# Optimization experiments

Measured on AMD Instinct MI355X. Metric: run time of the kernel, lower is better.

The kernel has to match this reference:

```python
import jax, jax.numpy as jnp
import numpy as np

N, D, C = 8192, 512, 1000


def setup_inputs() -> dict:
    key = jax.random.key(0)
    k1, k2, k3 = jax.random.split(key, 3)
    features = jax.random.normal(k1, (N, D), dtype=jnp.float32)
    centers = jax.random.normal(k2, (C, D), dtype=jnp.float32)
    labels = jax.random.randint(k3, (N,), 0, C, dtype=jnp.int64)
    return {"features": features, "centers": centers, "labels": labels}


def _l2_normalize(x, axis=1, eps=1e-12):
    # matches torch F.normalize(p=2): x / max(||x||, eps)
    norm = jnp.sqrt(jnp.sum(x * x, axis=axis, keepdims=True))
    return x / jnp.maximum(norm, eps)


def reference(features, centers, labels):
    f = _l2_normalize(features, axis=1)          # [N, D]
    c = _l2_normalize(centers, axis=1)           # [C, D]
    centers_batch = c[labels]                    # [N, D]
    pos_distances = 1.0 - jnp.sum(f * centers_batch, axis=1)      # [N]
    neg_distances = 1.0 - jnp.matmul(f, f.T)                       # [N, N]
    losses = pos_distances[:, None] - neg_distances                # [N, N]
    diff_class = labels[:, None] != labels[None, :]                # [N, N]
    valid = diff_class & (losses > 0.0)                            # [N, N]
    losses = jnp.where(valid, losses, 0.0)
    num_valid_pairs = jnp.sum(valid, axis=1)                       # [N]
    num_valid_pairs = jnp.where(num_valid_pairs > 0, num_valid_pairs, 1)
    sample_losses = jnp.sum(losses, axis=1) / num_valid_pairs.astype(losses.dtype)
    num_valid_samples = jnp.sum(sample_losses > 0.0)
    loss = jnp.sum(sample_losses)
    loss = jnp.where(num_valid_samples > 0,
                     loss / num_valid_samples.astype(loss.dtype), loss)
    return loss
```

## Files before the change

### kernel.cpp

```cpp
#include <hip/hip_runtime.h>
#include <hip/hip_bf16.h>
#include <hip/hip_fp8.h>
#include <stdint.h>
#include <math.h>

#define N_ROWS 8192
#define DIM    512
#define BM     128
#define BK     64
#define NB     (N_ROWS / BM)
#define NTRI   (NB * (NB + 1) / 2)
#define NKT    (DIM / BK)

typedef float f32x4 __attribute__((ext_vector_type(4)));
typedef long  lng2  __attribute__((ext_vector_type(2)));


__global__ __launch_bounds__(256) void k_prep(const float* __restrict__ feats,
                                              const float* __restrict__ centers,
                                              const int* __restrict__ labels,
                                              unsigned char* __restrict__ f_q,
                                              float* __restrict__ posdot,
                                              float* __restrict__ Ssum,
                                              int* __restrict__ Kcnt) {
    const int row = blockIdx.x;
    const int t = threadIdx.x;
    const float* src = feats + (size_t)row * DIM;
    float v0 = src[t], v1 = src[t + 256];
    float ss = v0 * v0 + v1 * v1;
#pragma unroll
    for (int m = 1; m < 64; m <<= 1) ss += __shfl_xor(ss, m, 64);
    __shared__ float red[12];
    const int lane = t & 63, wid = t >> 6;
    if (lane == 0) red[wid] = ss;
    __syncthreads();
    const float tot = red[0] + red[1] + red[2] + red[3];
    const float scale = 1.0f / fmaxf(sqrtf(tot), 1e-12f);
    const float n0 = v0 * scale, n1 = v1 * scale;
    {
        __hip_fp8_e4m3 q0(n0), q1(n1);
#pragma unroll
        for (int j = 0; j < 2; ++j) {
            const int k  = t + j * 256;
            const int kt = k >> 6, k6 = k & 63;
            const int h  = (k6 >> 5) & 1;
            const int u  = (k6 >> 3) & 3;
            const int pos = kt * 64 + u * 16 + h * 8 + (k6 & 7);
            const unsigned char qb = (j == 0) ? *reinterpret_cast<const unsigned char*>(&q0)
                                              : *reinterpret_cast<const unsigned char*>(&q1);
            f_q[(size_t)row * DIM + pos] = qb;
        }
    }

    const int lab = labels[row];
    const float* c = centers + (size_t)lab * DIM;
    const float c0 = c[t], c1 = c[t + 256];
    float cc = c0 * c0 + c1 * c1;
    float d  = n0 * c0 + n1 * c1;
#pragma unroll
    for (int m = 1; m < 64; m <<= 1) {
        cc += __shfl_xor(cc, m, 64);
        d  += __shfl_xor(d, m, 64);
    }
    if (lane == 0) { red[4 + wid] = cc; red[8 + wid] = d; }
    __syncthreads();
    if (t == 0) {
        const float ctot = red[4] + red[5] + red[6] + red[7];
        const float dtot = red[8] + red[9] + red[10] + red[11];
        posdot[row] = dtot / fmaxf(sqrtf(ctot), 1e-12f);
        Ssum[row] = 0.0f;
        Kcnt[row] = 0;
    }
}

__global__ __launch_bounds__(256) void k_pair(const unsigned char* __restrict__ f_q,
                                              const int* __restrict__ labels,
                                              const float* __restrict__ pd,
                                              float* __restrict__ Ssum,
                                              int* __restrict__ Kcnt) {
    __shared__ __align__(16) unsigned char sA[2][BM * BK];
    __shared__ __align__(16) unsigned char sB[2][BM * BK];
    __shared__ int   s_lr[BM];
    __shared__ int   s_lc[BM];
    __shared__ float s_pd[BM];
    __shared__ float s_pc[BM];

    const int tid  = threadIdx.x;
    const int lane = tid & 63;
    const int wid  = tid >> 6;
    const int wr   = wid >> 1, wc = wid & 1;

    const int t = blockIdx.x;
    int bi = (int)floor((2.0 * NB + 1.0 - sqrt((2.0 * NB + 1.0) * (2.0 * NB + 1.0) - 8.0 * (double)t)) * 0.5);
    while (bi * NB - bi * (bi - 1) / 2 > t) --bi;
    while ((bi + 1) * NB - (bi + 1) * bi / 2 <= t) ++bi;
    const int bj = bi + (t - (bi * NB - bi * (bi - 1) / 2));
    const int rowBase = bi * BM;
    const int colBase = bj * BM;
    const bool offdiag = (bi != bj);

    if (tid < BM) {
        s_lr[tid] = labels[rowBase + tid];
        s_pd[tid] = pd[rowBase + tid];
    } else {
        s_lc[tid - BM] = labels[colBase + tid - BM];
        s_pc[tid - BM] = pd[colBase + tid - BM];
    }

    f32x4 acc[4][4] = {};

    const int srow = lane >> 2;
    const int slu  = (lane & 3) ^ ((lane >> 3) & 3);

#define STAGE(KT, P)                                                                       \
    do {                                                                                   \
        const int k0_ = (KT) * BK;                                                         \
        _Pragma("unroll")                                                                  \
        for (int i_ = 0; i_ < 2; ++i_) {                                                   \
            const int ch_ = wid * 2 + i_;                                                  \
            const int r_  = ch_ * 16 + srow;                                               \
            const unsigned char* gA_ = f_q + ((size_t)(rowBase + r_) * DIM + k0_ + slu * 16); \
            const unsigned char* gB_ = f_q + ((size_t)(colBase + r_) * DIM + k0_ + slu * 16); \
            __builtin_amdgcn_global_load_lds(                                              \
                (const __attribute__((address_space(1))) void*)gA_,                        \
                (__attribute__((address_space(3))) void*)(&sA[P][ch_ * 1024]), 16, 0, 0);  \
            __builtin_amdgcn_global_load_lds(                                              \
                (const __attribute__((address_space(1))) void*)gB_,                        \
                (__attribute__((address_space(3))) void*)(&sB[P][ch_ * 1024]), 16, 0, 0);  \
        }                                                                                  \
    } while (0)

    const int pu = (lane >> 4) ^ ((lane >> 1) & 3);

#define COMPUTE(P)                                                                         \
    do {                                                                                   \
        lng2 aF[4], bF[4];                                                                 \
        _Pragma("unroll")                                                                  \
        for (int m = 0; m < 4; ++m) {                                                      \
            const int r = wr * 64 + m * 16 + (lane & 15);                                  \
            aF[m] = *(const lng2*)(&sA[P][r * 64 + pu * 16]);                              \
        }                                                                                  \
        _Pragma("unroll")                                                                  \
        for (int n = 0; n < 4; ++n) {                                                      \
            const int r = wc * 64 + n * 16 + (lane & 15);                                  \
            bF[n] = *(const lng2*)(&sB[P][r * 64 + pu * 16]);                              \
        }                                                                                  \
        _Pragma("unroll")                                                                  \
        for (int m = 0; m < 4; ++m)                                                        \
            _Pragma("unroll")                                                              \
            for (int n = 0; n < 4; ++n) {                                                  \
                acc[m][n] = __builtin_amdgcn_mfma_f32_16x16x32_fp8_fp8(aF[m].x, bF[n].x, acc[m][n], 0, 0, 0); \
                acc[m][n] = __builtin_amdgcn_mfma_f32_16x16x32_fp8_fp8(aF[m].y, bF[n].y, acc[m][n], 0, 0, 0); \
            }                                                                              \
    } while (0)

    STAGE(0, 0);
    __syncthreads();

    for (int kt = 0; kt < NKT - 1; ++kt) {
        const int cur = kt & 1;
        STAGE(kt + 1, cur ^ 1);
        COMPUTE(cur);
        __syncthreads();
    }
    COMPUTE((NKT - 1) & 1);

#undef STAGE
#undef COMPUTE

    float colS[4] = {0.f, 0.f, 0.f, 0.f};
    int   colK[4] = {0, 0, 0, 0};
    int   lcv[4]; float pcv[4];
#pragma unroll
    for (int n = 0; n < 4; ++n) {
        const int jl = wc * 64 + n * 16 + (lane & 15);
        lcv[n] = s_lc[jl];
        pcv[n] = s_pc[jl];
    }

#pragma unroll
    for (int m = 0; m < 4; ++m) {
        float rowS[4] = {0.f, 0.f, 0.f, 0.f};
        int   rowK[4] = {0, 0, 0, 0};
        const int rbase = wr * 64 + m * 16 + ((lane >> 4) << 2);
        int myLr[4]; float myPd[4];
#pragma unroll
        for (int g = 0; g < 4; ++g) { myLr[g] = s_lr[rbase + g]; myPd[g] = s_pd[rbase + g]; }
#pragma unroll
        for (int n = 0; n < 4; ++n) {
#pragma unroll
            for (int g = 0; g < 4; ++g) {
                const float s = acc[m][n][g];
                const bool diff = (myLr[g] != lcv[n]);
                if (diff && s > myPd[g]) { rowS[g] += (s - myPd[g]); rowK[g] += 1; }
                if (offdiag && diff && s > pcv[n]) { colS[n] += (s - pcv[n]); colK[n] += 1; }
            }
        }
#pragma unroll
        for (int g = 0; g < 4; ++g) {
#pragma unroll
            for (int d = 1; d < 16; d <<= 1) {
                rowS[g] += __shfl_xor(rowS[g], d, 64);
                rowK[g] += __shfl_xor(rowK[g], d, 64);
            }
        }
        if ((lane & 15) == 0) {
#pragma unroll
            for (int g = 0; g < 4; ++g) {
                const int r = rowBase + rbase + g;
                atomicAdd(&Ssum[r], rowS[g]);
                atomicAdd(&Kcnt[r], rowK[g]);
            }
        }
    }

    if (offdiag) {
#pragma unroll
        for (int n = 0; n < 4; ++n) {
#pragma unroll
            for (int d = 16; d < 64; d <<= 1) {
                colS[n] += __shfl_xor(colS[n], d, 64);
                colK[n] += __shfl_xor(colK[n], d, 64);
            }
        }
        if (lane < 16) {
#pragma unroll
            for (int n = 0; n < 4; ++n) {
                const int c = colBase + wc * 64 + n * 16 + lane;
                atomicAdd(&Ssum[c], colS[n]);
                atomicAdd(&Kcnt[c], colK[n]);
            }
        }
    }
}

__global__ __launch_bounds__(1024) void k_final(const float* __restrict__ Ssum,
                                                const int* __restrict__ Kcnt,
                                                float* __restrict__ out) {
    const int t = threadIdx.x;
    double sum = 0.0; int cnt = 0;
    for (int i = t; i < N_ROWS; i += 1024) {
        const int k = Kcnt[i];
        if (k > 0) { sum += (double)Ssum[i] / (double)k; cnt += 1; }
    }
#pragma unroll
    for (int d = 1; d < 64; d <<= 1) {
        sum += __shfl_xor(sum, d, 64);
        cnt += __shfl_xor(cnt, d, 64);
    }
    __shared__ double s_sum[16];
    __shared__ int    s_cnt[16];
    const int lane = t & 63, wid = t >> 6;
    if (lane == 0) { s_sum[wid] = sum; s_cnt[wid] = cnt; }
    __syncthreads();
    if (t == 0) {
        double ts = 0.0; int tc = 0;
#pragma unroll
        for (int w = 0; w < 16; ++w) { ts += s_sum[w]; tc += s_cnt[w]; }
        out[0] = (float)(tc > 0 ? ts / (double)tc : ts);
    }
}

extern "C" void kernel_launch(void* const* d_in, const int* in_sizes, int n_in,
                              void* d_out, int out_size, void* d_ws, size_t ws_size,
                              hipStream_t stream) {
    const float* features = (const float*)d_in[0];
    const float* centers  = (const float*)d_in[1];
    const int*   labels   = (const int*)d_in[2];
    float* out = (float*)d_out;

    char* ws = (char*)d_ws;
    unsigned char* f_q    = (unsigned char*)(ws);
    float*         posdot = (float*)(ws + 0x400000);
    float*         Ssum   = (float*)(ws + 0x400000 + 0x8000);
    int*           Kcnt   = (int*)  (ws + 0x400000 + 0x10000);

    k_prep<<<N_ROWS, 256, 0, stream>>>(features, centers, labels, f_q, posdot, Ssum, Kcnt);
    k_pair<<<NTRI, 256, 0, stream>>>(f_q, labels, posdot, Ssum, Kcnt);
    k_final<<<1, 1024, 0, stream>>>(Ssum, Kcnt, out);
}
```

Before: 92.19 us.

## Load MFMA fragments directly from global memory instead of LDS staging

Removes the double-buffered LDS staging (global_load_lds plus syncthreads per k-tile) and has each wave load its fp8 A/B fragments straight from global memory into registers, with the k-loop fully unrolled. The goal is to cut the LDS traffic and barrier cost, and to raise occupancy by freeing shared memory. In exchange, each tile row is fetched from global/L2 by two waves rather than once per block, and the loads are 16-byte strided accesses that lean on the cache, so memory-latency stalls may become exposed.

```diff
diff --git a/kernel.cpp b/kernel.cpp
--- a/kernel.cpp
+++ b/kernel.cpp
@@ -78,8 +78,6 @@
                                               const float* __restrict__ pd,
                                               float* __restrict__ Ssum,
                                               int* __restrict__ Kcnt) {
-    __shared__ __align__(16) unsigned char sA[2][BM * BK];
-    __shared__ __align__(16) unsigned char sB[2][BM * BK];
     __shared__ int   s_lr[BM];
     __shared__ int   s_lc[BM];
     __shared__ float s_pd[BM];
@@ -106,67 +104,30 @@
         s_lc[tid - BM] = labels[colBase + tid - BM];
         s_pc[tid - BM] = pd[colBase + tid - BM];
     }
+    __syncthreads();
 
     f32x4 acc[4][4] = {};
 
-    const int srow = lane >> 2;
-    const int slu  = (lane & 3) ^ ((lane >> 3) & 3);
-
-#define STAGE(KT, P)                                                                       \
-    do {                                                                                   \
-        const int k0_ = (KT) * BK;                                                         \
-        _Pragma("unroll")                                                                  \
-        for (int i_ = 0; i_ < 2; ++i_) {                                                   \
-            const int ch_ = wid * 2 + i_;                                                  \
-            const int r_  = ch_ * 16 + srow;                                               \
-            const unsigned char* gA_ = f_q + ((size_t)(rowBase + r_) * DIM + k0_ + slu * 16); \
-            const unsigned char* gB_ = f_q + ((size_t)(colBase + r_) * DIM + k0_ + slu * 16); \
-            __builtin_amdgcn_global_load_lds(                                              \
-                (const __attribute__((address_space(1))) void*)gA_,                        \
-                (__attribute__((address_space(3))) void*)(&sA[P][ch_ * 1024]), 16, 0, 0);  \
-            __builtin_amdgcn_global_load_lds(                                              \
-                (const __attribute__((address_space(1))) void*)gB_,                        \
-                (__attribute__((address_space(3))) void*)(&sB[P][ch_ * 1024]), 16, 0, 0);  \
-        }                                                                                  \
-    } while (0)
-
-    const int pu = (lane >> 4) ^ ((lane >> 1) & 3);
-
-#define COMPUTE(P)                                                                         \
-    do {                                                                                   \
-        lng2 aF[4], bF[4];                                                                 \
-        _Pragma("unroll")                                                                  \
-        for (int m = 0; m < 4; ++m) {                                                      \
-            const int r = wr * 64 + m * 16 + (lane & 15);                                  \
-            aF[m] = *(const lng2*)(&sA[P][r * 64 + pu * 16]);                              \
-        }                                                                                  \
-        _Pragma("unroll")                                                                  \
-        for (int n = 0; n < 4; ++n) {                                                      \
-            const int r = wc * 64 + n * 16 + (lane & 15);                                  \
-            bF[n] = *(const lng2*)(&sB[P][r * 64 + pu * 16]);                              \
-        }                                                                                  \
-        _Pragma("unroll")                                                                  \
-        for (int m = 0; m < 4; ++m)                                                        \
-            _Pragma("unroll")                                                              \
-            for (int n = 0; n < 4; ++n) {                                                  \
-                acc[m][n] = __builtin_amdgcn_mfma_f32_16x16x32_fp8_fp8(aF[m].x, bF[n].x, acc[m][n], 0, 0, 0); \
-                acc[m][n] = __builtin_amdgcn_mfma_f32_16x16x32_fp8_fp8(aF[m].y, bF[n].y, acc[m][n], 0, 0, 0); \
-            }                                                                              \
-    } while (0)
-
-    STAGE(0, 0);
-    __syncthreads();
-
-    for (int kt = 0; kt < NKT - 1; ++kt) {
-        const int cur = kt & 1;
-        STAGE(kt + 1, cur ^ 1);
-        COMPUTE(cur);
-        __syncthreads();
-    }
-    COMPUTE((NKT - 1) & 1);
-
-#undef STAGE
-#undef COMPUTE
+    const unsigned char* baseA = f_q + (size_t)(rowBase + wr * 64 + (lane & 15)) * DIM + (lane >> 4) * 16;
+    const unsigned char* baseB = f_q + (size_t)(colBase + wc * 64 + (lane & 15)) * DIM + (lane >> 4) * 16;
+
+#pragma unroll
+    for (int kt = 0; kt < NKT; ++kt) {
+        lng2 aF[4], bF[4];
+#pragma unroll
+        for (int m = 0; m < 4; ++m)
+            aF[m] = *(const lng2*)(baseA + (size_t)m * 16 * DIM + kt * BK);
+#pragma unroll
+        for (int n = 0; n < 4; ++n)
+            bF[n] = *(const lng2*)(baseB + (size_t)n * 16 * DIM + kt * BK);
+#pragma unroll
+        for (int m = 0; m < 4; ++m)
+#pragma unroll
+            for (int n = 0; n < 4; ++n) {
+                acc[m][n] = __builtin_amdgcn_mfma_f32_16x16x32_fp8_fp8(aF[m].x, bF[n].x, acc[m][n], 0, 0, 0);
+                acc[m][n] = __builtin_amdgcn_mfma_f32_16x16x32_fp8_fp8(aF[m].y, bF[n].y, acc[m][n], 0, 0, 0);
+            }
+    }
 
     float colS[4] = {0.f, 0.f, 0.f, 0.f};
     int   colK[4] = {0, 0, 0, 0};
```

Result: slower. 130.5 us (+41.5%).

## Use one wave per row in prep and fold final reduction into last pair block

Applied to the files above, without the earlier changes.

The prep kernel now handles four rows per block, one wavefront each. It uses vectorized float4 loads and a packed 8-byte fp8 store, which removes the shared-memory reductions and block barriers. The final reduction kernel is removed: every pair block increments a completion counter, and the last block to finish reduces Ssum/Kcnt and writes the loss. This saves a kernel launch and the small per-row prep blocks, at the cost of a threadfence and an atomic in every pair block plus a serial tail in the last block.

```diff
diff --git a/kernel.cpp b/kernel.cpp
--- a/kernel.cpp
+++ b/kernel.cpp
@@ -22,52 +22,51 @@
                                               unsigned char* __restrict__ f_q,
                                               float* __restrict__ posdot,
                                               float* __restrict__ Ssum,
-                                              int* __restrict__ Kcnt) {
-    const int row = blockIdx.x;
-    const int t = threadIdx.x;
-    const float* src = feats + (size_t)row * DIM;
-    float v0 = src[t], v1 = src[t + 256];
-    float ss = v0 * v0 + v1 * v1;
+                                              int* __restrict__ Kcnt,
+                                              unsigned int* __restrict__ done) {
+    const int tid  = threadIdx.x;
+    const int lane = tid & 63;
+    const int w    = tid >> 6;
+    const int row  = blockIdx.x * 4 + w;
+    if (blockIdx.x == 0 && tid == 0) *done = 0u;
+
+    const float* src = feats + (size_t)row * DIM + lane * 8;
+    const f32x4 v0 = *(const f32x4*)(src);
+    const f32x4 v1 = *(const f32x4*)(src + 4);
+    float ss = v0.x*v0.x + v0.y*v0.y + v0.z*v0.z + v0.w*v0.w
+             + v1.x*v1.x + v1.y*v1.y + v1.z*v1.z + v1.w*v1.w;
 #pragma unroll
     for (int m = 1; m < 64; m <<= 1) ss += __shfl_xor(ss, m, 64);
-    __shared__ float red[12];
-    const int lane = t & 63, wid = t >> 6;
-    if (lane == 0) red[wid] = ss;
-    __syncthreads();
-    const float tot = red[0] + red[1] + red[2] + red[3];
-    const float scale = 1.0f / fmaxf(sqrtf(tot), 1e-12f);
-    const float n0 = v0 * scale, n1 = v1 * scale;
-    {
-        __hip_fp8_e4m3 q0(n0), q1(n1);
-#pragma unroll
-        for (int j = 0; j < 2; ++j) {
-            const int k  = t + j * 256;
-            const int kt = k >> 6, k6 = k & 63;
-            const int h  = (k6 >> 5) & 1;
-            const int u  = (k6 >> 3) & 3;
-            const int pos = kt * 64 + u * 16 + h * 8 + (k6 & 7);
-            const unsigned char qb = (j == 0) ? *reinterpret_cast<const unsigned char*>(&q0)
-                                              : *reinterpret_cast<const unsigned char*>(&q1);
-            f_q[(size_t)row * DIM + pos] = qb;
-        }
-    }
+    const float scale = 1.0f / fmaxf(sqrtf(ss), 1e-12f);
+
+    float vals[8] = { v0.x*scale, v0.y*scale, v0.z*scale, v0.w*scale,
+                      v1.x*scale, v1.y*scale, v1.z*scale, v1.w*scale };
+    unsigned long long packed = 0ull;
+#pragma unroll
+    for (int j = 0; j < 8; ++j) {
+        __hip_fp8_e4m3 q(vals[j]);
+        packed |= (unsigned long long)(*reinterpret_cast<const unsigned char*>(&q)) << (8 * j);
+    }
+    const int k  = lane * 8;
+    const int kt = k >> 6, k6 = k & 63;
+    const int h  = (k6 >> 5) & 1, u = (k6 >> 3) & 3;
+    *reinterpret_cast<unsigned long long*>(f_q + (size_t)row * DIM + kt * 64 + u * 16 + h * 8) = packed;
 
     const int lab = labels[row];
-    const float* c = centers + (size_t)lab * DIM;
-    const float c0 = c[t], c1 = c[t + 256];
-    float cc = c0 * c0 + c1 * c1;
-    float d  = n0 * c0 + n1 * c1;
+    const float* c = centers + (size_t)lab * DIM + lane * 8;
+    const f32x4 c0 = *(const f32x4*)(c);
+    const f32x4 c1 = *(const f32x4*)(c + 4);
+    float cc = c0.x*c0.x + c0.y*c0.y + c0.z*c0.z + c0.w*c0.w
+             + c1.x*c1.x + c1.y*c1.y + c1.z*c1.z + c1.w*c1.w;
+    float d  = vals[0]*c0.x + vals[1]*c0.y + vals[2]*c0.z + vals[3]*c0.w
+             + vals[4]*c1.x + vals[5]*c1.y + vals[6]*c1.z + vals[7]*c1.w;
 #pragma unroll
     for (int m = 1; m < 64; m <<= 1) {
         cc += __shfl_xor(cc, m, 64);
         d  += __shfl_xor(d, m, 64);
     }
-    if (lane == 0) { red[4 + wid] = cc; red[8 + wid] = d; }
-    __syncthreads();
-    if (t == 0) {
-        const float ctot = red[4] + red[5] + red[6] + red[7];
-        const float dtot = red[8] + red[9] + red[10] + red[11];
-        posdot[row] = dtot / fmaxf(sqrtf(ctot), 1e-12f);
+    if (lane == 0) {
+        posdot[row] = d / fmaxf(sqrtf(cc), 1e-12f);
         Ssum[row] = 0.0f;
         Kcnt[row] = 0;
     }
@@ -77,7 +76,9 @@
                                               const int* __restrict__ labels,
                                               const float* __restrict__ pd,
                                               float* __restrict__ Ssum,
-                                              int* __restrict__ Kcnt) {
+                                              int* __restrict__ Kcnt,
+                                              unsigned int* __restrict__ done,
+                                              float* __restrict__ out) {
     __shared__ __align__(16) unsigned char sA[2][BM * BK];
     __shared__ __align__(16) unsigned char sB[2][BM * BK];
     __shared__ int   s_lr[BM];
@@ -232,32 +233,35 @@
             }
         }
     }
-}
-
-__global__ __launch_bounds__(1024) void k_final(const float* __restrict__ Ssum,
-                                                const int* __restrict__ Kcnt,
-                                                float* __restrict__ out) {
-    const int t = threadIdx.x;
-    double sum = 0.0; int cnt = 0;
-    for (int i = t; i < N_ROWS; i += 1024) {
-        const int k = Kcnt[i];
-        if (k > 0) { sum += (double)Ssum[i] / (double)k; cnt += 1; }
-    }
-#pragma unroll
-    for (int d = 1; d < 64; d <<= 1) {
-        sum += __shfl_xor(sum, d, 64);
-        cnt += __shfl_xor(cnt, d, 64);
-    }
-    __shared__ double s_sum[16];
-    __shared__ int    s_cnt[16];
-    const int lane = t & 63, wid = t >> 6;
-    if (lane == 0) { s_sum[wid] = sum; s_cnt[wid] = cnt; }
+
+    __threadfence();
+    __shared__ unsigned int s_last;
+    __shared__ double s_dsum[4];
+    __shared__ int    s_dcnt[4];
+    if (tid == 0) s_last = (atomicAdd(done, 1u) == (unsigned)(NTRI - 1)) ? 1u : 0u;
     __syncthreads();
-    if (t == 0) {
-        double ts = 0.0; int tc = 0;
-#pragma unroll
-        for (int w = 0; w < 16; ++w) { ts += s_sum[w]; tc += s_cnt[w]; }
-        out[0] = (float)(tc > 0 ? ts / (double)tc : ts);
+    if (s_last) {
+        double sum = 0.0; int cnt = 0;
+        for (int i = tid; i < N_ROWS; i += 256) {
+            const int k = __hip_atomic_load(&Kcnt[i], __ATOMIC_RELAXED, __HIP_MEMORY_SCOPE_AGENT);
+            if (k > 0) {
+                const float s = __hip_atomic_load(&Ssum[i], __ATOMIC_RELAXED, __HIP_MEMORY_SCOPE_AGENT);
+                sum += (double)s / (double)k;
+                cnt += 1;
+            }
+        }
+#pragma unroll
+        for (int d = 1; d < 64; d <<= 1) {
+            sum += __shfl_xor(sum, d, 64);
+            cnt += __shfl_xor(cnt, d, 64);
+        }
+        if (lane == 0) { s_dsum[wid] = sum; s_dcnt[wid] = cnt; }
+        __syncthreads();
+        if (tid == 0) {
+            const double ts = s_dsum[0] + s_dsum[1] + s_dsum[2] + s_dsum[3];
+            const int    tc = s_dcnt[0] + s_dcnt[1] + s_dcnt[2] + s_dcnt[3];
+            out[0] = (float)(tc > 0 ? ts / (double)tc : ts);
+        }
     }
 }
 
@@ -274,8 +278,8 @@
     float*         posdot = (float*)(ws + 0x400000);
     float*         Ssum   = (float*)(ws + 0x400000 + 0x8000);
     int*           Kcnt   = (int*)  (ws + 0x400000 + 0x10000);
-
-    k_prep<<<N_ROWS, 256, 0, stream>>>(features, centers, labels, f_q, posdot, Ssum, Kcnt);
-    k_pair<<<NTRI, 256, 0, stream>>>(f_q, labels, posdot, Ssum, Kcnt);
-    k_final<<<1, 1024, 0, stream>>>(Ssum, Kcnt, out);
+    unsigned int*  done   = (unsigned int*)(ws + 0x400000 + 0x18000);
+
+    k_prep<<<N_ROWS / 4, 256, 0, stream>>>(features, centers, labels, f_q, posdot, Ssum, Kcnt, done);
+    k_pair<<<NTRI, 256, 0, stream>>>(f_q, labels, posdot, Ssum, Kcnt, done, out);
 }
```

New measurement: 237.4 us. 2.58x slower.
